# Kernel tuning notes

Hardware: AMD Instinct MI355X
Metric: run time of the kernel (lower is better)

Reference implementation:

```python
import jax, jax.numpy as jnp
import numpy as np

B, S, D = 4, 2048, 1024  # batch, seq_len, model dim (= qk_dim = output_dim)


def setup_inputs() -> dict:
    key = jax.random.key(0)
    kq, kk, kv, kwq, kwk, kwv = jax.random.split(key, 6)
    q = jax.random.normal(kq, (B, S, D), dtype=jnp.float32)
    k = jax.random.normal(kk, (B, S, D), dtype=jnp.float32)
    v = jax.random.normal(kv, (B, S, D), dtype=jnp.float32)
    # causal mask, broadcast over batch
    mask = jnp.broadcast_to(jnp.tril(jnp.ones((S, S), dtype=bool)), (B, S, S))
    W_q = jax.random.uniform(kwq, (D, D), dtype=jnp.float32)
    W_k = jax.random.uniform(kwk, (D, D), dtype=jnp.float32)
    W_v = jax.random.uniform(kwv, (D, D), dtype=jnp.float32)
    return {"q": q, "k": k, "v": v, "mask": mask, "W_q": W_q, "W_k": W_k, "W_v": W_v}


def reference(q, k, v, mask, W_q, W_k, W_v):
    q1 = q @ W_q  # (B, S, D)
    k1 = k @ W_k  # (B, S, D)
    v1 = v @ W_v  # (B, S, D)
    qk = jnp.einsum('bij,bkj->bik', q1, k1)  # (B, S, S)
    qk = qk * jax.lax.rsqrt(float(k1.shape[-1]))
    neg_inf = jnp.finfo(jnp.float32).min
    qk = jnp.where(mask, qk, neg_inf)
    s = jax.nn.softmax(qk, axis=-1)
    return jnp.einsum('bij,bjk->bik', s, v1)
```

## Files before the change

kernel.cpp:

```cpp
#include <hip/hip_runtime.h>
#include <hip/hip_bf16.h>
#include <float.h>


typedef __attribute__((ext_vector_type(8))) short bf16x8;
typedef __attribute__((ext_vector_type(4))) float f32x4;

#define MFMA16 __builtin_amdgcn_mfma_f32_16x16x32_bf16

union U8 { bf16x8 v; unsigned w[4]; };

__device__ __forceinline__ ushort f2bf(float x) {
  union { float f; unsigned u; } v; v.f = x;
  unsigned r = v.u + 0x7fffu + ((v.u >> 16) & 1u);
  return (ushort)(r >> 16);
}
__device__ __forceinline__ float bf2f(ushort h) {
  union { unsigned u; float f; } v; v.u = ((unsigned)h) << 16;
  return v.f;
}
__device__ __forceinline__ void splitf(float x, ushort& hi, ushort& lo) {
  hi = f2bf(x);
  lo = f2bf(x - bf2f(hi));
}

__device__ __forceinline__ bf16x8 cvt8(const float* lp) {
  U8 H;
#pragma unroll
  for (int p = 0; p < 4; ++p) {
    const unsigned u0 = __float_as_uint(lp[2 * p]);
    const unsigned u1 = __float_as_uint(lp[2 * p + 1]);
    const unsigned r0 = (u0 + 0x7fffu + ((u0 >> 16) & 1u)) >> 16;
    const unsigned r1 = (u1 + 0x7fffu + ((u1 >> 16) & 1u)) & 0xffff0000u;
    H.w[p] = r0 | r1;
  }
  return H.v;
}

#define GLOAD16(gp, lp)                                                        \
  __builtin_amdgcn_global_load_lds(                                            \
      (const __attribute__((address_space(1))) void*)(gp),                     \
      (__attribute__((address_space(3))) void*)(lp), 16, 0, 0)

__device__ __forceinline__ void stage_bf16_32(const ushort* g, int pitch,
                                              ushort* lds, int w, int lane) {
#pragma unroll
  for (int i = 0; i < 2; ++i) {
    const int c = w * 2 + i;
    const int row = c * 16 + (lane >> 2);
    const int kp = (lane & 3) * 8;
    GLOAD16(g + (size_t)row * pitch + kp, lds + c * 512);
  }
}
__device__ __forceinline__ void stage_bf16_64(const ushort* g, int pitch,
                                              ushort* lds, int w, int lane) {
#pragma unroll
  for (int i = 0; i < 4; ++i) {
    const int c = w * 4 + i;
    const int row = c * 8 + (lane >> 3);
    const int kp = (lane & 7) * 8;
    GLOAD16(g + (size_t)row * pitch + kp, lds + c * 512);
  }
}
__device__ __forceinline__ void stage_f32_32(const float* g, int pitch,
                                             float* lds, int w, int lane) {
#pragma unroll
  for (int i = 0; i < 4; ++i) {
    const int c = w * 4 + i;
    const int row = c * 8 + (lane >> 3);
    const int kp = (lane & 7) * 4;
    GLOAD16(g + (size_t)row * pitch + kp, lds + c * 256);
  }
}

__global__ __launch_bounds__(256) void split_pre(
    const float* __restrict__ q, const float* __restrict__ k,
    ushort* __restrict__ qh, ushort* __restrict__ ql,
    ushort* __restrict__ kh, ushort* __restrict__ kl) {
  const float* X = blockIdx.y ? k : q;
  ushort* H = blockIdx.y ? kh : qh;
  ushort* L = blockIdx.y ? kl : ql;
  const int n4 = 2097152;
  for (int i = blockIdx.x * 256 + threadIdx.x; i < n4; i += 2048 * 256) {
    const float4 x = reinterpret_cast<const float4*>(X)[i];
    ushort h0, l0, h1, l1, h2, l2, h3, l3;
    splitf(x.x, h0, l0); splitf(x.y, h1, l1);
    splitf(x.z, h2, l2); splitf(x.w, h3, l3);
    reinterpret_cast<ushort4*>(H)[i] = ushort4{h0, h1, h2, h3};
    reinterpret_cast<ushort4*>(L)[i] = ushort4{l0, l1, l2, l3};
  }
}

__global__ __launch_bounds__(256) void wt_conv(
    const float* __restrict__ W0, const float* __restrict__ W1,
    const float* __restrict__ W2, ushort* __restrict__ Th0,
    ushort* __restrict__ Tl0, ushort* __restrict__ Th1,
    ushort* __restrict__ Tl1, ushort* __restrict__ Th2) {
  __shared__ float t[32][33];
  const int z = blockIdx.z;
  const float* W = z == 0 ? W0 : (z == 1 ? W1 : W2);
  ushort* Th = z == 0 ? Th0 : (z == 1 ? Th1 : Th2);
  ushort* Tl = z == 0 ? Tl0 : (z == 1 ? Tl1 : nullptr);
  const int bx = blockIdx.x, by = blockIdx.y;
  const int r = threadIdx.x >> 3, c4 = (threadIdx.x & 7) * 4;
  const float4 x =
      *reinterpret_cast<const float4*>(&W[(size_t)(bx * 32 + r) * 1024 + by * 32 + c4]);
  t[r][c4] = x.x; t[r][c4 + 1] = x.y; t[r][c4 + 2] = x.z; t[r][c4 + 3] = x.w;
  __syncthreads();
  ushort h[4], l[4];
#pragma unroll
  for (int j = 0; j < 4; ++j) splitf(t[c4 + j][r], h[j], l[j]);
  const size_t o = (size_t)(by * 32 + r) * 1024 + bx * 32 + c4;
  *reinterpret_cast<ushort4*>(&Th[o]) = ushort4{h[0], h[1], h[2], h[3]};
  if (Tl)
    *reinterpret_cast<ushort4*>(&Tl[o]) = ushort4{l[0], l[1], l[2], l[3]};
}

__global__ __launch_bounds__(256) void proj_qk(
    const ushort* __restrict__ Ah0, const ushort* __restrict__ Al0,
    const ushort* __restrict__ Ah1, const ushort* __restrict__ Al1,
    const ushort* __restrict__ Bh0, const ushort* __restrict__ Bl0,
    const ushort* __restrict__ Bh1, const ushort* __restrict__ Bl1,
    ushort* __restrict__ Oh0, ushort* __restrict__ Ol0,
    ushort* __restrict__ Oh1, ushort* __restrict__ Ol1) {
  __shared__ ushort Ahs[4096], Als[4096], Bhs[4096], Bls[4096];
  const int z = blockIdx.z;
  const ushort* Ah = z ? Ah1 : Ah0;
  const ushort* Al = z ? Al1 : Al0;
  const ushort* Bh = z ? Bh1 : Bh0;
  const ushort* Bl = z ? Bl1 : Bl0;
  ushort* Oh = z ? Oh1 : Oh0;
  ushort* Ol = z ? Ol1 : Ol0;
  const int tid = threadIdx.x, lane = tid & 63, w = tid >> 6;
  const int wr = w >> 1, wc = w & 1;
  const int lr = lane & 15, kg = lane >> 4;
  const int m0 = blockIdx.y * 128, n0 = blockIdx.x * 128;
  f32x4 acc[4][4] = {};

  for (int k0 = 0; k0 < 1024; k0 += 32) {
    stage_bf16_32(Ah + (size_t)m0 * 1024 + k0, 1024, Ahs, w, lane);
    stage_bf16_32(Al + (size_t)m0 * 1024 + k0, 1024, Als, w, lane);
    stage_bf16_32(Bh + (size_t)n0 * 1024 + k0, 1024, Bhs, w, lane);
    stage_bf16_32(Bl + (size_t)n0 * 1024 + k0, 1024, Bls, w, lane);
    __syncthreads();
    bf16x8 ah[4], al[4], bh[4], bl[4];
#pragma unroll
    for (int m = 0; m < 4; ++m) {
      ah[m] = *reinterpret_cast<bf16x8*>(&Ahs[(wr * 64 + m * 16 + lr) * 32 + kg * 8]);
      al[m] = *reinterpret_cast<bf16x8*>(&Als[(wr * 64 + m * 16 + lr) * 32 + kg * 8]);
    }
#pragma unroll
    for (int n = 0; n < 4; ++n) {
      bh[n] = *reinterpret_cast<bf16x8*>(&Bhs[(wc * 64 + n * 16 + lr) * 32 + kg * 8]);
      bl[n] = *reinterpret_cast<bf16x8*>(&Bls[(wc * 64 + n * 16 + lr) * 32 + kg * 8]);
    }
#pragma unroll
    for (int m = 0; m < 4; ++m)
#pragma unroll
      for (int n = 0; n < 4; ++n) {
        acc[m][n] = MFMA16(ah[m], bh[n], acc[m][n], 0, 0, 0);
        acc[m][n] = MFMA16(ah[m], bl[n], acc[m][n], 0, 0, 0);
        acc[m][n] = MFMA16(al[m], bh[n], acc[m][n], 0, 0, 0);
      }
    __syncthreads();
  }
#pragma unroll
  for (int m = 0; m < 4; ++m)
#pragma unroll
    for (int n = 0; n < 4; ++n)
#pragma unroll
      for (int reg = 0; reg < 4; ++reg) {
        const int gm = m0 + wr * 64 + m * 16 + kg * 4 + reg;
        const int gn = n0 + wc * 64 + n * 16 + lr;
        ushort h, l;
        splitf(acc[m][n][reg], h, l);
        Oh[(size_t)gm * 1024 + gn] = h;
        Ol[(size_t)gm * 1024 + gn] = l;
      }
}

__global__ __launch_bounds__(256) void proj_v(const ushort* __restrict__ Wvt,
                                              const float* __restrict__ V,
                                              ushort* __restrict__ v1t) {
  __shared__ ushort Ahs[4096];
  __shared__ float Bs[4096];
  const int tid = threadIdx.x, lane = tid & 63, w = tid >> 6;
  const int wr = w >> 1, wc = w & 1;
  const int lr = lane & 15, kg = lane >> 4;
  const int m0 = blockIdx.y * 128;
  const int n0 = blockIdx.x * 128;
  f32x4 acc[4][4] = {};

  for (int k0 = 0; k0 < 1024; k0 += 32) {
    stage_bf16_32(Wvt + (size_t)m0 * 1024 + k0, 1024, Ahs, w, lane);
    stage_f32_32(V + (size_t)n0 * 1024 + k0, 1024, Bs, w, lane);
    __syncthreads();
    bf16x8 ah[4], bh[4];
#pragma unroll
    for (int m = 0; m < 4; ++m)
      ah[m] = *reinterpret_cast<bf16x8*>(&Ahs[(wr * 64 + m * 16 + lr) * 32 + kg * 8]);
#pragma unroll
    for (int n = 0; n < 4; ++n)
      bh[n] = cvt8(&Bs[(wc * 64 + n * 16 + lr) * 32 + kg * 8]);
#pragma unroll
    for (int m = 0; m < 4; ++m)
#pragma unroll
      for (int n = 0; n < 4; ++n)
        acc[m][n] = MFMA16(ah[m], bh[n], acc[m][n], 0, 0, 0);
    __syncthreads();
  }
#pragma unroll
  for (int m = 0; m < 4; ++m)
#pragma unroll
    for (int n = 0; n < 4; ++n)
#pragma unroll
      for (int reg = 0; reg < 4; ++reg) {
        const int gm = m0 + wr * 64 + m * 16 + kg * 4 + reg;
        const int gn = n0 + wc * 64 + n * 16 + lr;
        const int b = gn >> 11, jj = gn & 2047;
        v1t[((size_t)b << 21) + (size_t)gm * 2048 + jj] = f2bf(acc[m][n][reg]);
      }
}

__global__ __launch_bounds__(256) void qk2(
    const ushort* __restrict__ q1h, const ushort* __restrict__ q1l,
    const ushort* __restrict__ k1h, const ushort* __restrict__ k1l,
    float* __restrict__ scoresA, float* __restrict__ scoresB) {
  __shared__ ushort Ahs[4096], Als[4096], Bhs[4096], Bls[4096];
  const int tid = threadIdx.x, lane = tid & 63, w = tid >> 6;
  const int wr = w >> 1, wc = w & 1;
  const int lr = lane & 15, kg = lane >> 4;
  const int b = blockIdx.y;
  const int kh0 = blockIdx.z * 512;
  int p = blockIdx.x, ti = 0, accp = 0;
  while (accp + ti + 1 <= p) { accp += ti + 1; ++ti; }
  const int tj = p - accp;
  const ushort* qh = q1h + ((size_t)b * 2048 + ti * 128) * 1024 + kh0;
  const ushort* ql = q1l + ((size_t)b * 2048 + ti * 128) * 1024 + kh0;
  const ushort* kh = k1h + ((size_t)b * 2048 + tj * 128) * 1024 + kh0;
  const ushort* kl = k1l + ((size_t)b * 2048 + tj * 128) * 1024 + kh0;
  f32x4 acc[4][4] = {};

  for (int k0 = 0; k0 < 512; k0 += 32) {
    stage_bf16_32(qh + k0, 1024, Ahs, w, lane);
    stage_bf16_32(ql + k0, 1024, Als, w, lane);
    stage_bf16_32(kh + k0, 1024, Bhs, w, lane);
    stage_bf16_32(kl + k0, 1024, Bls, w, lane);
    __syncthreads();
    bf16x8 ah[4], al[4], bh[4], bl[4];
#pragma unroll
    for (int m = 0; m < 4; ++m) {
      ah[m] = *reinterpret_cast<bf16x8*>(&Ahs[(wr * 64 + m * 16 + lr) * 32 + kg * 8]);
      al[m] = *reinterpret_cast<bf16x8*>(&Als[(wr * 64 + m * 16 + lr) * 32 + kg * 8]);
    }
#pragma unroll
    for (int n = 0; n < 4; ++n) {
      bh[n] = *reinterpret_cast<bf16x8*>(&Bhs[(wc * 64 + n * 16 + lr) * 32 + kg * 8]);
      bl[n] = *reinterpret_cast<bf16x8*>(&Bls[(wc * 64 + n * 16 + lr) * 32 + kg * 8]);
    }
#pragma unroll
    for (int m = 0; m < 4; ++m)
#pragma unroll
      for (int n = 0; n < 4; ++n) {
        acc[m][n] = MFMA16(ah[m], bh[n], acc[m][n], 0, 0, 0);
        acc[m][n] = MFMA16(ah[m], bl[n], acc[m][n], 0, 0, 0);
        acc[m][n] = MFMA16(al[m], bh[n], acc[m][n], 0, 0, 0);
      }
    __syncthreads();
  }
  const float sc = 0.03125f;
  float* st = (blockIdx.z ? scoresB : scoresA) + ((size_t)b * 136 + p) * 16384;
#pragma unroll
  for (int m = 0; m < 4; ++m)
#pragma unroll
    for (int n = 0; n < 4; ++n)
#pragma unroll
      for (int reg = 0; reg < 4; ++reg) {
        const int il = wr * 64 + m * 16 + kg * 4 + reg;
        const int jl = wc * 64 + n * 16 + lr;
        st[il * 128 + jl] = acc[m][n][reg] * sc;
      }
}

__global__ __launch_bounds__(256) void softmax_kernel(
    float* __restrict__ scoresA, const float* __restrict__ scoresB) {
  __shared__ float red[8];
  const int rb = blockIdx.x;
  const int b = rb >> 11, r = rb & 2047;
  const int ti = r >> 7, rl = r & 127, ncol = (ti + 1) * 128;
  const int valid = r + 1;
  const size_t tbase = ((size_t)b * 136 + (ti * (ti + 1)) / 2) * 16384;
  float* srowA = scoresA + tbase;
  const float* srowB = scoresB + tbase;
  const int tid = threadIdx.x, lane = tid & 63, w = tid >> 6;

  float vals[8];
  float mx = -FLT_MAX;
#pragma unroll
  for (int c = 0; c < 8; ++c) {
    const int j = tid + c * 256;
    const size_t o = (size_t)(j >> 7) * 16384 + rl * 128 + (j & 127);
    vals[c] = (j < valid) ? (srowA[o] + srowB[o]) : -FLT_MAX;
    mx = fmaxf(mx, vals[c]);
  }
#pragma unroll
  for (int o = 32; o; o >>= 1) mx = fmaxf(mx, __shfl_xor(mx, o));
  if (lane == 0) red[w] = mx;
  __syncthreads();
  mx = fmaxf(fmaxf(red[0], red[1]), fmaxf(red[2], red[3]));

  float ex[8];
  float sum = 0.f;
#pragma unroll
  for (int c = 0; c < 8; ++c) {
    const int j = tid + c * 256;
    ex[c] = (j < valid) ? __expf(vals[c] - mx) : 0.f;
    sum += ex[c];
  }
#pragma unroll
  for (int o = 32; o; o >>= 1) sum += __shfl_xor(sum, o);
  if (lane == 0) red[4 + w] = sum;
  __syncthreads();
  sum = red[4] + red[5] + red[6] + red[7];
  const float inv = 1.f / sum;
#pragma unroll
  for (int c = 0; c < 8; ++c) {
    const int j = tid + c * 256;
    if (j < ncol) {
      ushort* pt = reinterpret_cast<ushort*>(srowA + (size_t)(j >> 7) * 16384);
      pt[rl * 256 + (j & 127)] = f2bf(ex[c] * inv);
    }
  }
}

__global__ __launch_bounds__(256) void pv2(const float* __restrict__ scores,
                                           const ushort* __restrict__ v1t,
                                           float* __restrict__ out) {
  __shared__ ushort Ps[128 * 64], Vs[128 * 64];
  const int tid = threadIdx.x, lane = tid & 63, w = tid >> 6;
  const int wr = w >> 1, wc = w & 1;
  const int lr = lane & 15, kg = lane >> 4;
  const int b = blockIdx.z;
  const int ti = 15 - blockIdx.y;
  const int n0 = blockIdx.x * 128;
  const int tri_ti = (ti * (ti + 1)) / 2;
  const ushort* vbase = v1t + ((size_t)b << 21) + (size_t)n0 * 2048;
  const int kend = (ti + 1) * 128;
  f32x4 acc[4][4] = {};

  for (int k0 = 0; k0 < kend; k0 += 64) {
    const ushort* pt = reinterpret_cast<const ushort*>(
        scores + ((size_t)b * 136 + tri_ti + (k0 >> 7)) * 16384);
    stage_bf16_64(pt + (k0 & 64), 256, Ps, w, lane);
    stage_bf16_64(vbase + k0, 2048, Vs, w, lane);
    __syncthreads();
#pragma unroll
    for (int t2 = 0; t2 < 2; ++t2) {
      bf16x8 pa[4], vb[4];
#pragma unroll
      for (int m = 0; m < 4; ++m)
        pa[m] = *reinterpret_cast<bf16x8*>(
            &Ps[(wr * 64 + m * 16 + lr) * 64 + t2 * 32 + kg * 8]);
#pragma unroll
      for (int n = 0; n < 4; ++n)
        vb[n] = *reinterpret_cast<bf16x8*>(
            &Vs[(wc * 64 + n * 16 + lr) * 64 + t2 * 32 + kg * 8]);
#pragma unroll
      for (int m = 0; m < 4; ++m)
#pragma unroll
        for (int n = 0; n < 4; ++n)
          acc[m][n] = MFMA16(pa[m], vb[n], acc[m][n], 0, 0, 0);
    }
    __syncthreads();
  }
#pragma unroll
  for (int m = 0; m < 4; ++m)
#pragma unroll
    for (int n = 0; n < 4; ++n)
#pragma unroll
      for (int reg = 0; reg < 4; ++reg) {
        const int gm = ti * 128 + wr * 64 + m * 16 + kg * 4 + reg;
        const int gn = n0 + wc * 64 + n * 16 + lr;
        out[((size_t)b * 2048 + gm) * 1024 + gn] = acc[m][n][reg];
      }
}

extern "C" void kernel_launch(void* const* d_in, const int* in_sizes, int n_in,
                              void* d_out, int out_size, void* d_ws,
                              size_t ws_size, hipStream_t stream) {
  const float* q = (const float*)d_in[0];
  const float* k = (const float*)d_in[1];
  const float* v = (const float*)d_in[2];
  const float* Wq = (const float*)d_in[4];
  const float* Wk = (const float*)d_in[5];
  const float* Wv = (const float*)d_in[6];
  float* out = (float*)d_out;

  char* ws = (char*)d_ws;
  const size_t SCORES_T = 35651584;
  float* scoresA = (float*)ws;
  float* scoresB = (float*)(ws + SCORES_T);
  ushort* qsh = (ushort*)ws;
  ushort* qsl = qsh + 8388608;
  ushort* ksh = qsh + 2 * 8388608;
  ushort* ksl = qsh + 3 * 8388608;
  ushort* q1hi = (ushort*)(ws + 2 * SCORES_T);
  ushort* q1lo = q1hi + 8388608;
  ushort* k1hi = q1hi + 2 * 8388608;
  ushort* k1lo = q1hi + 3 * 8388608;
  ushort* v1t = (ushort*)(ws + 2 * SCORES_T);
  ushort* Wqth = (ushort*)(ws + 2 * SCORES_T + 67108864);
  ushort* Wqtl = Wqth + 1048576;
  ushort* Wkth = Wqth + 2097152;
  ushort* Wktl = Wqth + 3145728;
  ushort* Wvt  = Wqth + 4194304;
  const size_t need = 2 * SCORES_T + 67108864 + 10485760;
  if (ws_size < need) return;

  dim3 blk(256);
  wt_conv<<<dim3(32, 32, 3), blk, 0, stream>>>(Wq, Wk, Wv, Wqth, Wqtl, Wkth,
                                               Wktl, Wvt);
  split_pre<<<dim3(2048, 2), blk, 0, stream>>>(q, k, qsh, qsl, ksh, ksl);
  proj_qk<<<dim3(8, 64, 2), blk, 0, stream>>>(qsh, qsl, ksh, ksl, Wqth, Wqtl,
                                              Wkth, Wktl, q1hi, q1lo, k1hi,
                                              k1lo);
  qk2<<<dim3(136, 4, 2), blk, 0, stream>>>(q1hi, q1lo, k1hi, k1lo, scoresA,
                                           scoresB);
  softmax_kernel<<<dim3(8192), blk, 0, stream>>>(scoresA, scoresB);
  proj_v<<<dim3(64, 8), blk, 0, stream>>>(Wvt, v, v1t);
  pv2<<<dim3(8, 16, 4), blk, 0, stream>>>(scoresA, v1t, out);
}
```

Measured before the change: 350.6 us.

## Remap block indices for XCD-aware L2 locality and vectorize softmax accesses

```diff
diff --git a/kernel.cpp b/kernel.cpp
--- a/kernel.cpp
+++ b/kernel.cpp
@@ -124,7 +124,10 @@
     ushort* __restrict__ Oh0, ushort* __restrict__ Ol0,
     ushort* __restrict__ Oh1, ushort* __restrict__ Ol1) {
   __shared__ ushort Ahs[4096], Als[4096], Bhs[4096], Bls[4096];
-  const int z = blockIdx.z;
+  const int f = blockIdx.x;
+  const int xb = (f >> 3) & 7;
+  const int r = (f & 7) + ((f >> 6) << 3);
+  const int yb = r & 63, z = r >> 6;
   const ushort* Ah = z ? Ah1 : Ah0;
   const ushort* Al = z ? Al1 : Al0;
   const ushort* Bh = z ? Bh1 : Bh0;
@@ -134,7 +137,7 @@
   const int tid = threadIdx.x, lane = tid & 63, w = tid >> 6;
   const int wr = w >> 1, wc = w & 1;
   const int lr = lane & 15, kg = lane >> 4;
-  const int m0 = blockIdx.y * 128, n0 = blockIdx.x * 128;
+  const int m0 = yb * 128, n0 = xb * 128;
   f32x4 acc[4][4] = {};
 
   for (int k0 = 0; k0 < 1024; k0 += 32) {
@@ -184,11 +187,14 @@
                                               ushort* __restrict__ v1t) {
   __shared__ ushort Ahs[4096];
   __shared__ float Bs[4096];
+  const int f = blockIdx.x;
+  const int yb = (f >> 3) & 7;
+  const int xb = (f & 7) + ((f >> 6) << 3);
   const int tid = threadIdx.x, lane = tid & 63, w = tid >> 6;
   const int wr = w >> 1, wc = w & 1;
   const int lr = lane & 15, kg = lane >> 4;
-  const int m0 = blockIdx.y * 128;
-  const int n0 = blockIdx.x * 128;
+  const int m0 = yb * 128;
+  const int n0 = xb * 128;
   f32x4 acc[4][4] = {};
 
   for (int k0 = 0; k0 < 1024; k0 += 32) {
@@ -227,14 +233,18 @@
     const ushort* __restrict__ k1h, const ushort* __restrict__ k1l,
     float* __restrict__ scoresA, float* __restrict__ scoresB) {
   __shared__ ushort Ahs[4096], Als[4096], Bhs[4096], Bls[4096];
+  const int f = blockIdx.x;
+  const int s = (f & 7) * 136 + (f >> 3);
+  const int z = s / 544;
+  const int rem = s % 544;
+  const int b = rem / 136;
+  int p = rem % 136, ti = 0, accp = 0;
+  while (accp + ti + 1 <= p) { accp += ti + 1; ++ti; }
+  const int tj = p - accp;
   const int tid = threadIdx.x, lane = tid & 63, w = tid >> 6;
   const int wr = w >> 1, wc = w & 1;
   const int lr = lane & 15, kg = lane >> 4;
-  const int b = blockIdx.y;
-  const int kh0 = blockIdx.z * 512;
-  int p = blockIdx.x, ti = 0, accp = 0;
-  while (accp + ti + 1 <= p) { accp += ti + 1; ++ti; }
-  const int tj = p - accp;
+  const int kh0 = z * 512;
   const ushort* qh = q1h + ((size_t)b * 2048 + ti * 128) * 1024 + kh0;
   const ushort* ql = q1l + ((size_t)b * 2048 + ti * 128) * 1024 + kh0;
   const ushort* kh = k1h + ((size_t)b * 2048 + tj * 128) * 1024 + kh0;
@@ -269,7 +279,7 @@
     __syncthreads();
   }
   const float sc = 0.03125f;
-  float* st = (blockIdx.z ? scoresB : scoresA) + ((size_t)b * 136 + p) * 16384;
+  float* st = (z ? scoresB : scoresA) + ((size_t)b * 136 + p) * 16384;
 #pragma unroll
   for (int m = 0; m < 4; ++m)
 #pragma unroll
@@ -294,14 +304,20 @@
   const float* srowB = scoresB + tbase;
   const int tid = threadIdx.x, lane = tid & 63, w = tid >> 6;
 
-  float vals[8];
+  float vals[2][4];
   float mx = -FLT_MAX;
 #pragma unroll
-  for (int c = 0; c < 8; ++c) {
-    const int j = tid + c * 256;
+  for (int c = 0; c < 2; ++c) {
+    const int j = tid * 4 + c * 1024;
     const size_t o = (size_t)(j >> 7) * 16384 + rl * 128 + (j & 127);
-    vals[c] = (j < valid) ? (srowA[o] + srowB[o]) : -FLT_MAX;
-    mx = fmaxf(mx, vals[c]);
+    const float4 a = *reinterpret_cast<const float4*>(srowA + o);
+    const float4 bb = *reinterpret_cast<const float4*>(srowB + o);
+    vals[c][0] = (j + 0 < valid) ? a.x + bb.x : -FLT_MAX;
+    vals[c][1] = (j + 1 < valid) ? a.y + bb.y : -FLT_MAX;
+    vals[c][2] = (j + 2 < valid) ? a.z + bb.z : -FLT_MAX;
+    vals[c][3] = (j + 3 < valid) ? a.w + bb.w : -FLT_MAX;
+    mx = fmaxf(mx, fmaxf(fmaxf(vals[c][0], vals[c][1]),
+                         fmaxf(vals[c][2], vals[c][3])));
   }
 #pragma unroll
   for (int o = 32; o; o >>= 1) mx = fmaxf(mx, __shfl_xor(mx, o));
@@ -309,14 +325,16 @@
   __syncthreads();
   mx = fmaxf(fmaxf(red[0], red[1]), fmaxf(red[2], red[3]));
 
-  float ex[8];
+  float ex[2][4];
   float sum = 0.f;
 #pragma unroll
-  for (int c = 0; c < 8; ++c) {
-    const int j = tid + c * 256;
-    ex[c] = (j < valid) ? __expf(vals[c] - mx) : 0.f;
-    sum += ex[c];
-  }
+  for (int c = 0; c < 2; ++c)
+#pragma unroll
+    for (int e = 0; e < 4; ++e) {
+      const int j = tid * 4 + c * 1024 + e;
+      ex[c][e] = (j < valid) ? __expf(vals[c][e] - mx) : 0.f;
+      sum += ex[c][e];
+    }
 #pragma unroll
   for (int o = 32; o; o >>= 1) sum += __shfl_xor(sum, o);
   if (lane == 0) red[4 + w] = sum;
@@ -324,11 +342,14 @@
   sum = red[4] + red[5] + red[6] + red[7];
   const float inv = 1.f / sum;
 #pragma unroll
-  for (int c = 0; c < 8; ++c) {
-    const int j = tid + c * 256;
+  for (int c = 0; c < 2; ++c) {
+    const int j = tid * 4 + c * 1024;
     if (j < ncol) {
       ushort* pt = reinterpret_cast<ushort*>(srowA + (size_t)(j >> 7) * 16384);
-      pt[rl * 256 + (j & 127)] = f2bf(ex[c] * inv);
+      ushort4 pw;
+      pw.x = f2bf(ex[c][0] * inv); pw.y = f2bf(ex[c][1] * inv);
+      pw.z = f2bf(ex[c][2] * inv); pw.w = f2bf(ex[c][3] * inv);
+      *reinterpret_cast<ushort4*>(&pt[rl * 256 + (j & 127)]) = pw;
     }
   }
 }
@@ -337,12 +358,14 @@
                                            const ushort* __restrict__ v1t,
                                            float* __restrict__ out) {
   __shared__ ushort Ps[128 * 64], Vs[128 * 64];
+  const int fl = blockIdx.x;
+  const int s = (fl & 7) * 64 + (fl >> 3);
+  const int xb = s & 7, yb = (s >> 3) & 15, b = s >> 7;
   const int tid = threadIdx.x, lane = tid & 63, w = tid >> 6;
   const int wr = w >> 1, wc = w & 1;
   const int lr = lane & 15, kg = lane >> 4;
-  const int b = blockIdx.z;
-  const int ti = 15 - blockIdx.y;
-  const int n0 = blockIdx.x * 128;
+  const int ti = 15 - yb;
+  const int n0 = xb * 128;
   const int tri_ti = (ti * (ti + 1)) / 2;
   const ushort* vbase = v1t + ((size_t)b << 21) + (size_t)n0 * 2048;
   const int kend = (ti + 1) * 128;
@@ -421,12 +444,11 @@
   wt_conv<<<dim3(32, 32, 3), blk, 0, stream>>>(Wq, Wk, Wv, Wqth, Wqtl, Wkth,
                                                Wktl, Wvt);
   split_pre<<<dim3(2048, 2), blk, 0, stream>>>(q, k, qsh, qsl, ksh, ksl);
-  proj_qk<<<dim3(8, 64, 2), blk, 0, stream>>>(qsh, qsl, ksh, ksl, Wqth, Wqtl,
-                                              Wkth, Wktl, q1hi, q1lo, k1hi,
-                                              k1lo);
-  qk2<<<dim3(136, 4, 2), blk, 0, stream>>>(q1hi, q1lo, k1hi, k1lo, scoresA,
-                                           scoresB);
+  proj_qk<<<dim3(1024), blk, 0, stream>>>(qsh, qsl, ksh, ksl, Wqth, Wqtl,
+                                          Wkth, Wktl, q1hi, q1lo, k1hi, k1lo);
+  qk2<<<dim3(1088), blk, 0, stream>>>(q1hi, q1lo, k1hi, k1lo, scoresA,
+                                      scoresB);
   softmax_kernel<<<dim3(8192), blk, 0, stream>>>(scoresA, scoresB);
-  proj_v<<<dim3(64, 8), blk, 0, stream>>>(Wvt, v, v1t);
-  pv2<<<dim3(8, 16, 4), blk, 0, stream>>>(scoresA, v1t, out);
-}
+  proj_v<<<dim3(512), blk, 0, stream>>>(Wvt, v, v1t);
+  pv2<<<dim3(512), blk, 0, stream>>>(scoresA, v1t, out);
+}
```

After: 314.9 us. 10.2% less time.
